# Optimization experiments

Hardware: AMD Instinct MI355X
Metric: run time of the kernel (lower is better)

The kernel has to match this reference:

```python
import jax, jax.numpy as jnp
import numpy as np

B, N, F, C, L = 8, 1024, 256, 256, 4


def setup_inputs() -> dict:
    key = jax.random.key(0)
    k1, k2, k3 = jax.random.split(key, 3)
    V = jax.random.normal(k1, (B, N, F), dtype=jnp.float32)
    A = jax.random.uniform(k2, (B, N, N, L), dtype=jnp.float32)
    # learned relational weights: (L+1, C, F); index 0 corresponds to the identity (self) edge
    h_weights = jax.random.normal(k3, (L + 1, C, F), dtype=jnp.float32) * 0.05
    return {"V": V, "A": A, "h_weights": h_weights}


def reference(V, A, h_weights):
    # out[b,i,c] = relu( sum_{l,j,f} A_aug[b,i,j,l] * h[l,c,f] * V[b,j,f] )
    # where A_aug = concat(I, A) on the last axis. We avoid materializing the
    # (B, N*C, N*F) intermediate of the naive impl by projecting V first.
    VW = jnp.einsum('bjf,lcf->bljc', V, h_weights)          # (B, L+1, N, C)
    # identity edge (l=0) contributes VW[:,0] directly; remaining L edge types aggregate over A
    out = VW[:, 0] + jnp.einsum('bijl,bljc->bic', A, VW[:, 1:])  # (B, N, C)
    return jax.nn.relu(out)
```

## Files before the change

### kernel.cpp

```cpp
#include <hip/hip_runtime.h>


typedef float          f32x4  __attribute__((ext_vector_type(4)));
typedef __bf16         bf16x8 __attribute__((ext_vector_type(8)));
typedef unsigned short u16x4  __attribute__((ext_vector_type(4)));
typedef unsigned int   u32x4  __attribute__((ext_vector_type(4)));

#define DEV __device__ __forceinline__

DEV void glds16(const void* g, void* l) {
  __builtin_amdgcn_global_load_lds((const __attribute__((address_space(1))) void*)g,
                                   (__attribute__((address_space(3))) void*)l,
                                   16, 0, 0);
}

DEV void cvt8(__bf16* d, f32x4 u, f32x4 v) {
  bf16x8 o;
  o[0]=(__bf16)u[0]; o[1]=(__bf16)u[1]; o[2]=(__bf16)u[2]; o[3]=(__bf16)u[3];
  o[4]=(__bf16)v[0]; o[5]=(__bf16)v[1]; o[6]=(__bf16)v[2]; o[7]=(__bf16)v[3];
  *(bf16x8*)d = o;
}

DEV bf16x8 cvt8r(f32x4 u, f32x4 v) {
  bf16x8 o;
  o[0]=(__bf16)u[0]; o[1]=(__bf16)u[1]; o[2]=(__bf16)u[2]; o[3]=(__bf16)u[3];
  o[4]=(__bf16)v[0]; o[5]=(__bf16)v[1]; o[6]=(__bf16)v[2]; o[7]=(__bf16)v[3];
  return o;
}

DEV unsigned short bfbits(float x) {
  return __builtin_bit_cast(unsigned short, (__bf16)x);
}

__global__ __launch_bounds__(512, 2)
void k1_vw(const float* __restrict__ Vg, const float* __restrict__ Hg,
           unsigned short* __restrict__ W2t, float* __restrict__ VW0)
{
  __shared__ __attribute__((aligned(16))) __bf16 Vs[2][128*64];
  __shared__ __attribute__((aligned(16))) __bf16 Hs[2][320*64];

  const int tid  = threadIdx.x;
  const int lane = tid & 63;
  const int wid  = tid >> 6;
  const int wj   = wid >> 1;
  const int wc   = wid & 1;
  const int li   = lane & 15;
  const int lg   = lane >> 4;

  const int p    = blockIdx.x;
  const int b    = p & 7;
  const int rest = p >> 3;
  const int ct   = rest & 3;
  const int jt   = rest >> 2;
  const int j0   = jt * 128;
  const int c0   = ct * 64;

  const float* sptr[7];
  int sdst[7];
#pragma unroll
  for (int r = 0; r < 2; ++r) {
    int n = r*512 + tid, row = n >> 3, q = n & 7;
    sptr[r] = Vg + (size_t)(b*1024 + j0 + row)*256 + q*8;
    sdst[r] = row*64 + ((q ^ (row & 7))*8);
  }
#pragma unroll
  for (int r = 0; r < 5; ++r) {
    int n = r*512 + tid, row = n >> 3, q = n & 7;
    int l = row >> 6, cl = row & 63;
    sptr[2+r] = Hg + (size_t)(l*256 + c0 + cl)*256 + q*8;
    sdst[2+r] = row*64 + ((q ^ (row & 7))*8);
  }

  f32x4 acc[5][2][2];
#pragma unroll
  for (int l=0;l<5;l++)
#pragma unroll
    for (int x=0;x<2;x++)
#pragma unroll
      for (int y=0;y<2;y++) acc[l][x][y] = (f32x4){0.f,0.f,0.f,0.f};

  {
    f32x4 sa[14];
#pragma unroll
    for (int i=0;i<7;i++) { sa[2*i] = *(const f32x4*)(sptr[i]); sa[2*i+1] = *(const f32x4*)(sptr[i]+4); }
#pragma unroll
    for (int i=0;i<7;i++) {
      __bf16* d = (i < 2) ? &Vs[0][sdst[i]] : &Hs[0][sdst[i]];
      cvt8(d, sa[2*i], sa[2*i+1]);
    }
  }
  __syncthreads();

  int cur = 0;
#pragma unroll 1
  for (int t = 0; t < 4; ++t) {
    const int nxt = cur ^ 1;
    f32x4 sa[14];
    if (t < 3) {
      const int ko = (t+1)*64;
#pragma unroll
      for (int i=0;i<7;i++) { sa[2*i] = *(const f32x4*)(sptr[i]+ko); sa[2*i+1] = *(const f32x4*)(sptr[i]+ko+4); }
    }
    const __bf16* Vsc = &Vs[cur][0];
    const __bf16* Hsc = &Hs[cur][0];
#pragma unroll
    for (int ks = 0; ks < 2; ++ks) {
      bf16x8 hf[10], vf[2];
#pragma unroll
      for (int l=0;l<5;l++)
#pragma unroll
        for (int cm=0;cm<2;cm++) {
          int row = l*64 + wc*32 + cm*16 + li;
          int ch  = (ks*4 + lg) ^ (row & 7);
          hf[l*2+cm] = *(const bf16x8*)(Hsc + row*64 + ch*8);
        }
#pragma unroll
      for (int jn=0;jn<2;jn++) {
        int row = wj*32 + jn*16 + li;
        int ch  = (ks*4 + lg) ^ (row & 7);
        vf[jn] = *(const bf16x8*)(Vsc + row*64 + ch*8);
      }
#pragma unroll
      for (int l=0;l<5;l++)
#pragma unroll
        for (int cm=0;cm<2;cm++)
#pragma unroll
          for (int jn=0;jn<2;jn++)
            acc[l][cm][jn] = __builtin_amdgcn_mfma_f32_16x16x32_bf16(
                hf[l*2+cm], vf[jn], acc[l][cm][jn], 0, 0, 0);
    }
    if (t < 3) {
#pragma unroll
      for (int i=0;i<7;i++) {
        __bf16* d = (i < 2) ? &Vs[nxt][sdst[i]] : &Hs[nxt][sdst[i]];
        cvt8(d, sa[2*i], sa[2*i+1]);
      }
    }
    __syncthreads();
    cur = nxt;
  }

#pragma unroll
  for (int cm=0;cm<2;cm++)
#pragma unroll
    for (int r=0;r<4;r++) {
      const int c = c0 + wc*32 + cm*16 + lg*4 + r;
#pragma unroll
      for (int jn=0;jn<2;jn++) {
        const int j = j0 + wj*32 + jn*16 + li;
        u16x4 pk;
        pk[0] = bfbits(acc[1][cm][jn][r]);
        pk[1] = bfbits(acc[2][cm][jn][r]);
        pk[2] = bfbits(acc[3][cm][jn][r]);
        pk[3] = bfbits(acc[4][cm][jn][r]);
        *(u16x4*)(W2t + (size_t)(b*256 + c)*4096 + (size_t)j*4) = pk;
        VW0[(size_t)(b*1024 + j)*256 + c] = acc[0][cm][jn][r];
      }
    }
}

#define K2_FENCE() do {                                          \
    asm volatile("s_waitcnt lgkmcnt(0)" ::: "memory");           \
    __builtin_amdgcn_sched_barrier(0);                           \
    __builtin_amdgcn_s_barrier();                                \
    __builtin_amdgcn_sched_barrier(0);                           \
  } while (0)

__global__ __launch_bounds__(512, 2)
void k2_gemm(const float* __restrict__ Ag, const unsigned short* __restrict__ W2t,
             unsigned short* __restrict__ part)
{
  __shared__ __attribute__((aligned(16))) __bf16 As[2][128*64];
  __shared__ __attribute__((aligned(16))) __bf16 Bs[2][256*64];

  const int tid  = threadIdx.x;
  const int lane = tid & 63;
  const int wid  = tid >> 6;
  const int wi   = wid >> 2;
  const int wc   = wid & 3;
  const int li   = lane & 15;
  const int lg   = lane >> 4;
  const int ls   = li & 7;

  const int p    = blockIdx.x;
  const int b    = p & 7;
  const int rest = p >> 3;
  const int kt   = rest & 3;
  const int it   = rest >> 2;

  const int i0 = it*128;
  const int k0 = kt*1024;

  const int ar = tid >> 2, aq = tid & 3, as_ = ar & 7;
  const float* asrc = Ag + (size_t)(b*1024 + i0 + ar)*4096 + k0;
  const int awo0 = ar*64 + ((aq     ^ as_)*8);
  const int awo1 = ar*64 + (((aq+4) ^ as_)*8);
  const int ago0 = aq*8;
  const int ago1 = aq*8 + 32;

  const int br = tid >> 1, h = tid & 1, bs_ = br & 7;
  const unsigned short* bsrc = W2t + (size_t)(b*256 + br)*4096 + k0;
  int bwo[4], bgo[4];
#pragma unroll
  for (int j=0;j<4;j++) {
    bwo[j] = br*64 + (((4*h+j) ^ bs_)*8);
    bgo[j] = (4*h+j)*8;
  }

  f32x4 acc[4][4];
#pragma unroll
  for (int m=0;m<4;m++)
#pragma unroll
    for (int n=0;n<4;n++) acc[m][n] = (f32x4){0.f,0.f,0.f,0.f};

  f32x4 aE0,aE1,aE2,aE3, aO0,aO1,aO2,aO3;
  u32x4 bE0,bE1,bE2,bE3, bO0,bO1,bO2,bO3;

#define K2_LOAD(S, t) do {                                                   \
    const float* _ap = asrc + (t)*64;                                        \
    a##S##0 = *(const f32x4*)(_ap + ago0);                                   \
    a##S##1 = *(const f32x4*)(_ap + ago0 + 4);                               \
    a##S##2 = *(const f32x4*)(_ap + ago1);                                   \
    a##S##3 = *(const f32x4*)(_ap + ago1 + 4);                               \
    const unsigned short* _bp = bsrc + (t)*64;                               \
    b##S##0 = *(const u32x4*)(_bp + bgo[0]);                                 \
    b##S##1 = *(const u32x4*)(_bp + bgo[1]);                                 \
    b##S##2 = *(const u32x4*)(_bp + bgo[2]);                                 \
    b##S##3 = *(const u32x4*)(_bp + bgo[3]);                                 \
  } while (0)

#define K2_DSW(S, X) do {                                                    \
    *(bf16x8*)(&As[X][awo0]) = cvt8r(a##S##0, a##S##1);                      \
    *(bf16x8*)(&As[X][awo1]) = cvt8r(a##S##2, a##S##3);                      \
    *(u32x4*)(&Bs[X][bwo[0]]) = b##S##0;                                     \
    *(u32x4*)(&Bs[X][bwo[1]]) = b##S##1;                                     \
    *(u32x4*)(&Bs[X][bwo[2]]) = b##S##2;                                     \
    *(u32x4*)(&Bs[X][bwo[3]]) = b##S##3;                                     \
  } while (0)

#define K2_COMP(X) do {                                                      \
    _Pragma("unroll")                                                        \
    for (int kk=0;kk<2;kk++) {                                               \
      bf16x8 af[4];                                                          \
      _Pragma("unroll")                                                      \
      for (int m=0;m<4;m++) {                                                \
        int row = wi*64 + m*16 + li;                                         \
        af[m] = *(const bf16x8*)(&As[X][row*64 + (((kk*4+lg) ^ ls)*8)]);     \
      }                                                                      \
      _Pragma("unroll")                                                      \
      for (int np=0;np<2;np++) {                                             \
        bf16x8 bf0, bf1;                                                     \
        {                                                                    \
          int row0 = wc*64 + (np*2  )*16 + li;                               \
          int row1 = wc*64 + (np*2+1)*16 + li;                               \
          bf0 = *(const bf16x8*)(&Bs[X][row0*64 + (((kk*4+lg) ^ ls)*8)]);    \
          bf1 = *(const bf16x8*)(&Bs[X][row1*64 + (((kk*4+lg) ^ ls)*8)]);    \
        }                                                                    \
        __builtin_amdgcn_s_setprio(1);                                       \
        _Pragma("unroll")                                                    \
        for (int m=0;m<4;m++) {                                              \
          acc[m][np*2  ] = __builtin_amdgcn_mfma_f32_16x16x32_bf16(          \
              af[m], bf0, acc[m][np*2  ], 0, 0, 0);                          \
          acc[m][np*2+1] = __builtin_amdgcn_mfma_f32_16x16x32_bf16(          \
              af[m], bf1, acc[m][np*2+1], 0, 0, 0);                          \
        }                                                                    \
        __builtin_amdgcn_s_setprio(0);                                       \
      }                                                                      \
    }                                                                        \
  } while (0)

  K2_LOAD(E, 0);
  K2_LOAD(O, 1);
  K2_DSW(E, 0);
  K2_FENCE();

#pragma unroll 1
  for (int u = 0; u < 7; ++u) {
    K2_LOAD(E, 2*u+2);
    K2_DSW(O, 1);
    K2_COMP(0);
    K2_FENCE();

    K2_LOAD(O, 2*u+3);
    K2_DSW(E, 0);
    K2_COMP(1);
    K2_FENCE();
  }
  K2_DSW(O, 1);
  K2_COMP(0);
  K2_FENCE();
  K2_COMP(1);

#undef K2_LOAD
#undef K2_DSW
#undef K2_COMP

  unsigned short* pb = part + (size_t)kt*2097152u + (size_t)(b*1024 + i0)*256;
#pragma unroll
  for (int m=0;m<4;m++)
#pragma unroll
    for (int r=0;r<4;r++) {
      const int il = wi*64 + m*16 + lg*4 + r;
#pragma unroll
      for (int n=0;n<4;n++) {
        const int cl = wc*64 + n*16 + li;
        pb[(size_t)il*256 + cl] = bfbits(acc[m][n][r]);
      }
    }
}

__global__ __launch_bounds__(256)
void k3_reduce(const unsigned short* __restrict__ part, const float* __restrict__ VW0,
               float* __restrict__ out)
{
  const size_t i8 = ((size_t)blockIdx.x*256 + threadIdx.x)*8;
  f32x4 s0 = *(const f32x4*)(VW0 + i8);
  f32x4 s1 = *(const f32x4*)(VW0 + i8 + 4);
#pragma unroll
  for (int q=0;q<4;q++) {
    u32x4 u = *(const u32x4*)(part + (size_t)q*2097152u + i8);
    s0[0] += __uint_as_float(u[0] << 16);  s0[1] += __uint_as_float(u[0] & 0xffff0000u);
    s0[2] += __uint_as_float(u[1] << 16);  s0[3] += __uint_as_float(u[1] & 0xffff0000u);
    s1[0] += __uint_as_float(u[2] << 16);  s1[1] += __uint_as_float(u[2] & 0xffff0000u);
    s1[2] += __uint_as_float(u[3] << 16);  s1[3] += __uint_as_float(u[3] & 0xffff0000u);
  }
#pragma unroll
  for (int e=0;e<4;e++){ s0[e] = fmaxf(s0[e],0.f); s1[e] = fmaxf(s1[e],0.f); }
  *(f32x4*)(out + i8)     = s0;
  *(f32x4*)(out + i8 + 4) = s1;
}

extern "C" void kernel_launch(void* const* d_in, const int* in_sizes, int n_in,
                              void* d_out, int out_size, void* d_ws, size_t ws_size,
                              hipStream_t stream) {
  const float* Vg = (const float*)d_in[0];
  const float* Ag = (const float*)d_in[1];
  const float* Hg = (const float*)d_in[2];
  float* out = (float*)d_out;

  if (ws_size < 41943040u) return;
  char* ws = (char*)d_ws;
  unsigned short* W2t  = (unsigned short*)(ws);
  float*          VW0  = (float*)(ws + 16777216u);
  unsigned short* part = (unsigned short*)(ws + 16777216u + 8388608u);

  k1_vw    <<<dim3(256),  dim3(512), 0, stream>>>(Vg, Hg, W2t, VW0);
  k2_gemm  <<<dim3(256),  dim3(512), 0, stream>>>(Ag, W2t, part);
  k3_reduce<<<dim3(1024), dim3(256), 0, stream>>>(part, VW0, out);
}
```

Baseline: 51.46 us.

## Split k2 GEMM tile along C into 128x128 blocks with 256 threads

The k2 GEMM block tile shrinks from 128x256 (512 threads) to 128x128 (256 threads), and the grid doubles to 512 blocks with a new c-tile index. Each thread now loads twice as much A per stage, and LDS per block drops because the B tile is halved. The aim is more blocks per CU and better occupancy or load balance. The cost is that each A row tile, which is the large fp32 input, is now read and converted twice, once per c-tile, roughly doubling A traffic.

Result: slower. 67.79 us (+31.7%).

```diff
diff --git a/kernel.cpp b/kernel.cpp
--- a/kernel.cpp
+++ b/kernel.cpp
@@ -7,12 +7,6 @@
 typedef unsigned int   u32x4  __attribute__((ext_vector_type(4)));
 
 #define DEV __device__ __forceinline__
-
-DEV void glds16(const void* g, void* l) {
-  __builtin_amdgcn_global_load_lds((const __attribute__((address_space(1))) void*)g,
-                                   (__attribute__((address_space(3))) void*)l,
-                                   16, 0, 0);
-}
 
 DEV void cvt8(__bf16* d, f32x4 u, f32x4 v) {
   bf16x8 o;
@@ -166,18 +160,18 @@
     __builtin_amdgcn_sched_barrier(0);                           \
   } while (0)
 
-__global__ __launch_bounds__(512, 2)
+__global__ __launch_bounds__(256, 2)
 void k2_gemm(const float* __restrict__ Ag, const unsigned short* __restrict__ W2t,
              unsigned short* __restrict__ part)
 {
   __shared__ __attribute__((aligned(16))) __bf16 As[2][128*64];
-  __shared__ __attribute__((aligned(16))) __bf16 Bs[2][256*64];
+  __shared__ __attribute__((aligned(16))) __bf16 Bs[2][128*64];
 
   const int tid  = threadIdx.x;
   const int lane = tid & 63;
   const int wid  = tid >> 6;
-  const int wi   = wid >> 2;
-  const int wc   = wid & 3;
+  const int wi   = wid >> 1;
+  const int wc   = wid & 1;
   const int li   = lane & 15;
   const int lg   = lane >> 4;
   const int ls   = li & 7;
@@ -185,27 +179,25 @@
   const int p    = blockIdx.x;
   const int b    = p & 7;
   const int rest = p >> 3;
-  const int kt   = rest & 3;
-  const int it   = rest >> 2;
+  const int ct   = rest & 1;
+  const int kt   = (rest >> 1) & 3;
+  const int it   = rest >> 3;
 
   const int i0 = it*128;
+  const int c0 = ct*128;
   const int k0 = kt*1024;
 
-  const int ar = tid >> 2, aq = tid & 3, as_ = ar & 7;
-  const float* asrc = Ag + (size_t)(b*1024 + i0 + ar)*4096 + k0;
-  const int awo0 = ar*64 + ((aq     ^ as_)*8);
-  const int awo1 = ar*64 + (((aq+4) ^ as_)*8);
-  const int ago0 = aq*8;
-  const int ago1 = aq*8 + 32;
-
-  const int br = tid >> 1, h = tid & 1, bs_ = br & 7;
-  const unsigned short* bsrc = W2t + (size_t)(b*256 + br)*4096 + k0;
-  int bwo[4], bgo[4];
-#pragma unroll
-  for (int j=0;j<4;j++) {
-    bwo[j] = br*64 + (((4*h+j) ^ bs_)*8);
-    bgo[j] = (4*h+j)*8;
-  }
+  const int ar = tid >> 1, ah = tid & 1, as_ = ar & 7;
+  const float* asrc = Ag + (size_t)(b*1024 + i0 + ar)*4096 + k0 + ah*32;
+  int awo[4];
+#pragma unroll
+  for (int j=0;j<4;j++) awo[j] = ar*64 + (((4*ah+j) ^ as_)*8);
+
+  const int br = tid >> 1, hb = tid & 1, bs_ = br & 7;
+  const unsigned short* bsrc = W2t + (size_t)(b*256 + c0 + br)*4096 + k0 + hb*32;
+  int bwo[4];
+#pragma unroll
+  for (int j=0;j<4;j++) bwo[j] = br*64 + (((4*hb+j) ^ bs_)*8);
 
   f32x4 acc[4][4];
 #pragma unroll
@@ -213,25 +205,31 @@
 #pragma unroll
     for (int n=0;n<4;n++) acc[m][n] = (f32x4){0.f,0.f,0.f,0.f};
 
-  f32x4 aE0,aE1,aE2,aE3, aO0,aO1,aO2,aO3;
+  f32x4 aE0,aE1,aE2,aE3,aE4,aE5,aE6,aE7, aO0,aO1,aO2,aO3,aO4,aO5,aO6,aO7;
   u32x4 bE0,bE1,bE2,bE3, bO0,bO1,bO2,bO3;
 
 #define K2_LOAD(S, t) do {                                                   \
     const float* _ap = asrc + (t)*64;                                        \
-    a##S##0 = *(const f32x4*)(_ap + ago0);                                   \
-    a##S##1 = *(const f32x4*)(_ap + ago0 + 4);                               \
-    a##S##2 = *(const f32x4*)(_ap + ago1);                                   \
-    a##S##3 = *(const f32x4*)(_ap + ago1 + 4);                               \
+    a##S##0 = *(const f32x4*)(_ap     );                                     \
+    a##S##1 = *(const f32x4*)(_ap +  4);                                     \
+    a##S##2 = *(const f32x4*)(_ap +  8);                                     \
+    a##S##3 = *(const f32x4*)(_ap + 12);                                     \
+    a##S##4 = *(const f32x4*)(_ap + 16);                                     \
+    a##S##5 = *(const f32x4*)(_ap + 20);                                     \
+    a##S##6 = *(const f32x4*)(_ap + 24);                                     \
+    a##S##7 = *(const f32x4*)(_ap + 28);                                     \
     const unsigned short* _bp = bsrc + (t)*64;                               \
-    b##S##0 = *(const u32x4*)(_bp + bgo[0]);                                 \
-    b##S##1 = *(const u32x4*)(_bp + bgo[1]);                                 \
-    b##S##2 = *(const u32x4*)(_bp + bgo[2]);                                 \
-    b##S##3 = *(const u32x4*)(_bp + bgo[3]);                                 \
+    b##S##0 = *(const u32x4*)(_bp     );                                     \
+    b##S##1 = *(const u32x4*)(_bp +  8);                                     \
+    b##S##2 = *(const u32x4*)(_bp + 16);                                     \
+    b##S##3 = *(const u32x4*)(_bp + 24);                                     \
   } while (0)
 
 #define K2_DSW(S, X) do {                                                    \
-    *(bf16x8*)(&As[X][awo0]) = cvt8r(a##S##0, a##S##1);                      \
-    *(bf16x8*)(&As[X][awo1]) = cvt8r(a##S##2, a##S##3);                      \
+    *(bf16x8*)(&As[X][awo[0]]) = cvt8r(a##S##0, a##S##1);                    \
+    *(bf16x8*)(&As[X][awo[1]]) = cvt8r(a##S##2, a##S##3);                    \
+    *(bf16x8*)(&As[X][awo[2]]) = cvt8r(a##S##4, a##S##5);                    \
+    *(bf16x8*)(&As[X][awo[3]]) = cvt8r(a##S##6, a##S##7);                    \
     *(u32x4*)(&Bs[X][bwo[0]]) = b##S##0;                                     \
     *(u32x4*)(&Bs[X][bwo[1]]) = b##S##1;                                     \
     *(u32x4*)(&Bs[X][bwo[2]]) = b##S##2;                                     \
@@ -295,7 +293,7 @@
 #undef K2_DSW
 #undef K2_COMP
 
-  unsigned short* pb = part + (size_t)kt*2097152u + (size_t)(b*1024 + i0)*256;
+  unsigned short* pb = part + (size_t)kt*2097152u + (size_t)(b*1024 + i0)*256 + c0;
 #pragma unroll
   for (int m=0;m<4;m++)
 #pragma unroll
@@ -345,6 +343,6 @@
   unsigned short* part = (unsigned short*)(ws + 16777216u + 8388608u);
 
   k1_vw    <<<dim3(256),  dim3(512), 0, stream>>>(Vg, Hg, W2t, VW0);
-  k2_gemm  <<<dim3(256),  dim3(512), 0, stream>>>(Ag, W2t, part);
+  k2_gemm  <<<dim3(512),  dim3(256), 0, stream>>>(Ag, W2t, part);
   k3_reduce<<<dim3(1024), dim3(256), 0, stream>>>(part, VW0, out);
 }
```

## Deepen k2 register prefetch to three stages and remap k3 block order

Applied to the files above, without the earlier changes.

The GEMM main loop now keeps three register sets of global loads (P/Q/R) in flight instead of two, so each tile load is issued two iterations before its LDS store. This is meant to hide more global-memory latency behind MFMA compute, at the cost of more VGPRs and possibly lower occupancy. The reduce kernel also maps block indices so that consecutive blocks walk across batches, which changes the memory access order. The unused global_load_lds helper is removed.

Measured after the change: 51.92 us. Within noise of the previous version (+0.9%).

```diff
diff --git a/kernel.cpp b/kernel.cpp
--- a/kernel.cpp
+++ b/kernel.cpp
@@ -7,12 +7,6 @@
 typedef unsigned int   u32x4  __attribute__((ext_vector_type(4)));
 
 #define DEV __device__ __forceinline__
-
-DEV void glds16(const void* g, void* l) {
-  __builtin_amdgcn_global_load_lds((const __attribute__((address_space(1))) void*)g,
-                                   (__attribute__((address_space(3))) void*)l,
-                                   16, 0, 0);
-}
 
 DEV void cvt8(__bf16* d, f32x4 u, f32x4 v) {
   bf16x8 o;
@@ -213,8 +207,8 @@
 #pragma unroll
     for (int n=0;n<4;n++) acc[m][n] = (f32x4){0.f,0.f,0.f,0.f};
 
-  f32x4 aE0,aE1,aE2,aE3, aO0,aO1,aO2,aO3;
-  u32x4 bE0,bE1,bE2,bE3, bO0,bO1,bO2,bO3;
+  f32x4 aP0,aP1,aP2,aP3, aQ0,aQ1,aQ2,aQ3, aR0,aR1,aR2,aR3;
+  u32x4 bP0,bP1,bP2,bP3, bQ0,bQ1,bQ2,bQ3, bR0,bR1,bR2,bR3;
 
 #define K2_LOAD(S, t) do {                                                   \
     const float* _ap = asrc + (t)*64;                                        \
@@ -269,26 +263,25 @@
     }                                                                        \
   } while (0)
 
-  K2_LOAD(E, 0);
-  K2_LOAD(O, 1);
-  K2_DSW(E, 0);
+  K2_LOAD(P, 0);
+  K2_LOAD(Q, 1);
+  K2_LOAD(R, 2);
+  K2_DSW(P, 0);
   K2_FENCE();
 
 #pragma unroll 1
-  for (int u = 0; u < 7; ++u) {
-    K2_LOAD(E, 2*u+2);
-    K2_DSW(O, 1);
-    K2_COMP(0);
-    K2_FENCE();
-
-    K2_LOAD(O, 2*u+3);
-    K2_DSW(E, 0);
-    K2_COMP(1);
-    K2_FENCE();
-  }
-  K2_DSW(O, 1);
-  K2_COMP(0);
-  K2_FENCE();
+  for (int u = 0; u < 2; ++u) {
+    const int t6 = u*6;
+    K2_LOAD(P, t6+3);  K2_DSW(Q, 1);  K2_COMP(0);  K2_FENCE();
+    K2_LOAD(Q, t6+4);  K2_DSW(R, 0);  K2_COMP(1);  K2_FENCE();
+    K2_LOAD(R, t6+5);  K2_DSW(P, 1);  K2_COMP(0);  K2_FENCE();
+    K2_LOAD(P, t6+6);  K2_DSW(Q, 0);  K2_COMP(1);  K2_FENCE();
+    K2_LOAD(Q, t6+7);  K2_DSW(R, 1);  K2_COMP(0);  K2_FENCE();
+    K2_LOAD(R, t6+8);  K2_DSW(P, 0);  K2_COMP(1);  K2_FENCE();
+  }
+  K2_LOAD(P, 15);  K2_DSW(Q, 1);  K2_COMP(0);  K2_FENCE();
+  K2_DSW(R, 0);    K2_COMP(1);    K2_FENCE();
+  K2_DSW(P, 1);    K2_COMP(0);    K2_FENCE();
   K2_COMP(1);
 
 #undef K2_LOAD
@@ -313,7 +306,10 @@
 void k3_reduce(const unsigned short* __restrict__ part, const float* __restrict__ VW0,
                float* __restrict__ out)
 {
-  const size_t i8 = ((size_t)blockIdx.x*256 + threadIdx.x)*8;
+  const int g   = blockIdx.x;
+  const int b   = g & 7;
+  const int off = g >> 3;
+  const size_t i8 = (size_t)b*262144u + (size_t)off*2048u + (size_t)threadIdx.x*8;
   f32x4 s0 = *(const f32x4*)(VW0 + i8);
   f32x4 s1 = *(const f32x4*)(VW0 + i8 + 4);
 #pragma unroll
```

## Enlarge GEMM tiles to 1024 threads, deepen split-K, load B via global_load_lds

Applied to the files above, without the earlier changes.

The aggregation GEMM now uses 1024-thread blocks with 256-row A tiles and splits K into eight 512-wide chunks instead of four. The B operand is copied straight from global memory into LDS with global_load_lds, with the XOR swizzle applied on the source side. Register staging of B is dropped and the waits are refined to vmcnt-based partial waits. The reduce kernel now sums eight bf16 partials. This raises reuse of B per block and overlaps loads with MFMA work, at the cost of twice the partial-sum traffic, a larger workspace, and heavy LDS and register pressure under the tighter launch bounds.

Result: slower. 70.93 us (+37.8%).

```diff
diff --git a/kernel.cpp b/kernel.cpp
--- a/kernel.cpp
+++ b/kernel.cpp
@@ -159,18 +159,11 @@
     }
 }
 
-#define K2_FENCE() do {                                          \
-    asm volatile("s_waitcnt lgkmcnt(0)" ::: "memory");           \
-    __builtin_amdgcn_sched_barrier(0);                           \
-    __builtin_amdgcn_s_barrier();                                \
-    __builtin_amdgcn_sched_barrier(0);                           \
-  } while (0)
-
-__global__ __launch_bounds__(512, 2)
+__global__ __launch_bounds__(1024, 4)
 void k2_gemm(const float* __restrict__ Ag, const unsigned short* __restrict__ W2t,
              unsigned short* __restrict__ part)
 {
-  __shared__ __attribute__((aligned(16))) __bf16 As[2][128*64];
+  __shared__ __attribute__((aligned(16))) __bf16 As[2][256*64];
   __shared__ __attribute__((aligned(16))) __bf16 Bs[2][256*64];
 
   const int tid  = threadIdx.x;
@@ -185,11 +178,11 @@
   const int p    = blockIdx.x;
   const int b    = p & 7;
   const int rest = p >> 3;
-  const int kt   = rest & 3;
-  const int it   = rest >> 2;
-
-  const int i0 = it*128;
-  const int k0 = kt*1024;
+  const int kt   = rest & 7;
+  const int it   = rest >> 3;
+
+  const int i0 = it*256;
+  const int k0 = kt*512;
 
   const int ar = tid >> 2, aq = tid & 3, as_ = ar & 7;
   const float* asrc = Ag + (size_t)(b*1024 + i0 + ar)*4096 + k0;
@@ -198,14 +191,11 @@
   const int ago0 = aq*8;
   const int ago1 = aq*8 + 32;
 
-  const int br = tid >> 1, h = tid & 1, bs_ = br & 7;
-  const unsigned short* bsrc = W2t + (size_t)(b*256 + br)*4096 + k0;
-  int bwo[4], bgo[4];
-#pragma unroll
-  for (int j=0;j<4;j++) {
-    bwo[j] = br*64 + (((4*h+j) ^ bs_)*8);
-    bgo[j] = (4*h+j)*8;
-  }
+  const int brow = tid >> 3, bq = tid & 7, bs_ = brow & 7;
+  const unsigned short* bsrc0 = W2t + (size_t)(b*256 +       brow)*4096 + k0 + ((bq ^ bs_)*8);
+  const unsigned short* bsrc1 = W2t + (size_t)(b*256 + 128 + brow)*4096 + k0 + ((bq ^ bs_)*8);
+  const int bd0 = wid*512;
+  const int bd1 = 8192 + wid*512;
 
   f32x4 acc[4][4];
 #pragma unroll
@@ -214,28 +204,23 @@
     for (int n=0;n<4;n++) acc[m][n] = (f32x4){0.f,0.f,0.f,0.f};
 
   f32x4 aE0,aE1,aE2,aE3, aO0,aO1,aO2,aO3;
-  u32x4 bE0,bE1,bE2,bE3, bO0,bO1,bO2,bO3;
-
-#define K2_LOAD(S, t) do {                                                   \
+
+#define K2_LOADA(S, t) do {                                                  \
     const float* _ap = asrc + (t)*64;                                        \
     a##S##0 = *(const f32x4*)(_ap + ago0);                                   \
     a##S##1 = *(const f32x4*)(_ap + ago0 + 4);                               \
     a##S##2 = *(const f32x4*)(_ap + ago1);                                   \
     a##S##3 = *(const f32x4*)(_ap + ago1 + 4);                               \
-    const unsigned short* _bp = bsrc + (t)*64;                               \
-    b##S##0 = *(const u32x4*)(_bp + bgo[0]);                                 \
-    b##S##1 = *(const u32x4*)(_bp + bgo[1]);                                 \
-    b##S##2 = *(const u32x4*)(_bp + bgo[2]);                                 \
-    b##S##3 = *(const u32x4*)(_bp + bgo[3]);                                 \
-  } while (0)
-
-#define K2_DSW(S, X) do {                                                    \
+  } while (0)
+
+#define K2_GLDSB(t, X) do {                                                  \
+    glds16(bsrc0 + (t)*64, &Bs[X][bd0]);                                     \
+    glds16(bsrc1 + (t)*64, &Bs[X][bd1]);                                     \
+  } while (0)
+
+#define K2_DSWA(S, X) do {                                                   \
     *(bf16x8*)(&As[X][awo0]) = cvt8r(a##S##0, a##S##1);                      \
     *(bf16x8*)(&As[X][awo1]) = cvt8r(a##S##2, a##S##3);                      \
-    *(u32x4*)(&Bs[X][bwo[0]]) = b##S##0;                                     \
-    *(u32x4*)(&Bs[X][bwo[1]]) = b##S##1;                                     \
-    *(u32x4*)(&Bs[X][bwo[2]]) = b##S##2;                                     \
-    *(u32x4*)(&Bs[X][bwo[3]]) = b##S##3;                                     \
   } while (0)
 
 #define K2_COMP(X) do {                                                      \
@@ -269,31 +254,51 @@
     }                                                                        \
   } while (0)
 
-  K2_LOAD(E, 0);
-  K2_LOAD(O, 1);
-  K2_DSW(E, 0);
-  K2_FENCE();
+#define K2_BARSB() do {                                                      \
+    __builtin_amdgcn_sched_barrier(0);                                       \
+    __builtin_amdgcn_s_barrier();                                            \
+    __builtin_amdgcn_sched_barrier(0);                                       \
+  } while (0)
+
+  K2_LOADA(E, 0);
+  K2_GLDSB(0, 0);
+  K2_DSWA(E, 0);
+  K2_LOADA(O, 1);
+  asm volatile("s_waitcnt lgkmcnt(0)" ::: "memory");
+  asm volatile("s_waitcnt vmcnt(4)"  ::: "memory");
+  K2_BARSB();
 
 #pragma unroll 1
-  for (int u = 0; u < 7; ++u) {
-    K2_LOAD(E, 2*u+2);
-    K2_DSW(O, 1);
+  for (int u = 0; u < 3; ++u) {
+    K2_GLDSB(2*u+1, 1);
+    K2_LOADA(E, 2*u+2);
     K2_COMP(0);
-    K2_FENCE();
-
-    K2_LOAD(O, 2*u+3);
-    K2_DSW(E, 0);
+    K2_DSWA(O, 1);
+    asm volatile("s_waitcnt lgkmcnt(0)" ::: "memory");
+    asm volatile("s_waitcnt vmcnt(4)"  ::: "memory");
+    K2_BARSB();
+
+    K2_GLDSB(2*u+2, 0);
+    K2_LOADA(O, 2*u+3);
     K2_COMP(1);
-    K2_FENCE();
-  }
-  K2_DSW(O, 1);
+    K2_DSWA(E, 0);
+    asm volatile("s_waitcnt lgkmcnt(0)" ::: "memory");
+    asm volatile("s_waitcnt vmcnt(4)"  ::: "memory");
+    K2_BARSB();
+  }
+  K2_GLDSB(7, 1);
   K2_COMP(0);
-  K2_FENCE();
+  K2_DSWA(O, 1);
+  asm volatile("s_waitcnt lgkmcnt(0)" ::: "memory");
+  asm volatile("s_waitcnt vmcnt(0)"  ::: "memory");
+  K2_BARSB();
   K2_COMP(1);
 
-#undef K2_LOAD
-#undef K2_DSW
+#undef K2_LOADA
+#undef K2_GLDSB
+#undef K2_DSWA
 #undef K2_COMP
+#undef K2_BARSB
 
   unsigned short* pb = part + (size_t)kt*2097152u + (size_t)(b*1024 + i0)*256;
 #pragma unroll
@@ -313,11 +318,14 @@
 void k3_reduce(const unsigned short* __restrict__ part, const float* __restrict__ VW0,
                float* __restrict__ out)
 {
-  const size_t i8 = ((size_t)blockIdx.x*256 + threadIdx.x)*8;
+  const int g   = blockIdx.x;
+  const int b   = g & 7;
+  const int off = g >> 3;
+  const size_t i8 = (size_t)b*262144u + (size_t)off*2048u + (size_t)threadIdx.x*8;
   f32x4 s0 = *(const f32x4*)(VW0 + i8);
   f32x4 s1 = *(const f32x4*)(VW0 + i8 + 4);
 #pragma unroll
-  for (int q=0;q<4;q++) {
+  for (int q=0;q<8;q++) {
     u32x4 u = *(const u32x4*)(part + (size_t)q*2097152u + i8);
     s0[0] += __uint_as_float(u[0] << 16);  s0[1] += __uint_as_float(u[0] & 0xffff0000u);
     s0[2] += __uint_as_float(u[1] << 16);  s0[3] += __uint_as_float(u[1] & 0xffff0000u);
@@ -338,13 +346,13 @@
   const float* Hg = (const float*)d_in[2];
   float* out = (float*)d_out;
 
-  if (ws_size < 41943040u) return;
+  if (ws_size < 58720256u) return;
   char* ws = (char*)d_ws;
   unsigned short* W2t  = (unsigned short*)(ws);
   float*          VW0  = (float*)(ws + 16777216u);
   unsigned short* part = (unsigned short*)(ws + 16777216u + 8388608u);
 
-  k1_vw    <<<dim3(256),  dim3(512), 0, stream>>>(Vg, Hg, W2t, VW0);
-  k2_gemm  <<<dim3(256),  dim3(512), 0, stream>>>(Ag, W2t, part);
-  k3_reduce<<<dim3(1024), dim3(256), 0, stream>>>(part, VW0, out);
-}
+  k1_vw    <<<dim3(256),  dim3(512),  0, stream>>>(Vg, Hg, W2t, VW0);
+  k2_gemm  <<<dim3(256),  dim3(1024), 0, stream>>>(Ag, W2t, part);
+  k3_reduce<<<dim3(1024), dim3(256),  0, stream>>>(part, VW0, out);
+}
```
